# Kernel tuning notes

Hardware: AMD Instinct MI355X
Metric: run time of the kernel (lower is better)

The kernel has to match this reference:

```python
import jax, jax.numpy as jnp
import numpy as np

DEPTH = 4  # truncation depth from init_kwargs


def restricted_exp(dx, depth):
    # exp(dx) in truncated tensor algebra: level k = dx^{\otimes k} / k!
    terms = [dx]
    for k in range(2, depth + 1):
        terms.append(jnp.tensordot(terms[-1], dx, axes=0) / k)
    return tuple(terms)


def chen_mult(a, b, depth):
    # Chen's relation: c_k = a_k + b_k + sum_{i=1}^{k-1} a_i \otimes b_{k-i}
    out = []
    for k in range(1, depth + 1):
        term = a[k - 1] + b[k - 1]
        for i in range(1, k):
            term = term + jnp.tensordot(a[i - 1], b[k - i - 1], axes=0)
        out.append(term)
    return tuple(out)


def signature(path, depth):
    inc = path[1:] - path[:-1]  # [L-1, D] path increments
    carry0 = restricted_exp(inc[0], depth)

    def step(carry, dx):
        return chen_mult(carry, restricted_exp(dx, depth), depth), None

    sig, _ = jax.lax.scan(step, carry0, inc[1:])
    # flatten=True: concat levels 1..depth -> [D + D^2 + ... + D^depth]
    return jnp.concatenate([t.reshape(-1) for t in sig])


def setup_inputs() -> dict:
    key = jax.random.key(0)
    path = jax.random.normal(key, (8192, 8), dtype=jnp.float32)
    return {"path": path}


def reference(path):
    return signature(path, DEPTH)
```

## Files before the change

kernel.cpp:

```cpp
#include <hip/hip_runtime.h>

#define SIGLEN 4680
#define S1OFF 0
#define S2OFF 8
#define S3OFF 72
#define S4OFF 584
#define NCHUNK 256
#define NG 16
#define MAXLEN 128
#define LROW 592

struct SigRegs { float s4[16]; float a1, a2, a30, a31; };

__device__ __forceinline__ int s3off(int c) {
  return S3OFF + 4 * (c ^ ((c >> 4) & 7));
}

__device__ __forceinline__ void load_sig(SigRegs& A, const float* __restrict__ B,
                                         int i_idx, int t) {
  const float4* p4 = (const float4*)(B + S4OFF + 16 * t);
#pragma unroll
  for (int r = 0; r < 4; ++r) {
    const float4 v = p4[r];
    A.s4[4 * r] = v.x; A.s4[4 * r + 1] = v.y; A.s4[4 * r + 2] = v.z; A.s4[4 * r + 3] = v.w;
  }
  A.a1 = B[S1OFF + i_idx];
  A.a2 = B[S2OFF + (t >> 2)];
  const float2 a3i = *(const float2*)(B + S3OFF + 2 * t);
  A.a30 = a3i.x; A.a31 = a3i.y;
}

__device__ __forceinline__ void store_sig(const SigRegs& A, float* __restrict__ o,
                                          int i_idx, int t) {
  if ((t & 31) == 0) o[S1OFF + i_idx] = A.a1;
  if ((t & 3) == 0) o[S2OFF + (t >> 2)] = A.a2;
  *(float2*)(o + S3OFF + 2 * t) = make_float2(A.a30, A.a31);
  float4* o4 = (float4*)(o + S4OFF + 16 * t);
#pragma unroll
  for (int r = 0; r < 4; ++r)
    o4[r] = make_float4(A.s4[4 * r], A.s4[4 * r + 1], A.s4[4 * r + 2], A.s4[4 * r + 3]);
}

__device__ __forceinline__ void fold_lds(SigRegs& A, const float* __restrict__ R,
                                         const float4* __restrict__ q4,
                                         int i_idx, int j_idx, int k0, int t) {
  const float4 b1lo = *(const float4*)(R + S1OFF);
  const float4 b1hi = *(const float4*)(R + S1OFF + 4);
  const float b1i = R[S1OFF + i_idx];
  const float b1j = R[S1OFF + j_idx];
  const float2 b1k = *(const float2*)(R + S1OFF + k0);
  const float b2own = R[S2OFF + (t >> 2)];
  const float2 b2p = *(const float2*)(R + S2OFF + ((2 * t) & 63));
  const float2 b3p = *(const float2*)(R + s3off(t >> 1) + 2 * (t & 1));
  const float4* q2 = (const float4*)(R + S2OFF + 16 * (t & 3));
#pragma unroll
  for (int r = 0; r < 4; ++r) {
    const float4 v2 = q2[r];
    const float4 v3 = *(const float4*)(R + s3off(4 * (t & 31) + r));
    const float4 v4 = q4[r];
    const float a3v = (r < 2) ? A.a30 : A.a31;
    const float4 bb = (r & 1) ? b1hi : b1lo;
    A.s4[4 * r + 0] += v4.x + A.a1 * v3.x + A.a2 * v2.x + a3v * bb.x;
    A.s4[4 * r + 1] += v4.y + A.a1 * v3.y + A.a2 * v2.y + a3v * bb.y;
    A.s4[4 * r + 2] += v4.z + A.a1 * v3.z + A.a2 * v2.z + a3v * bb.z;
    A.s4[4 * r + 3] += v4.w + A.a1 * v3.w + A.a2 * v2.w + a3v * bb.w;
  }
  A.a30 += b3p.x + A.a1 * b2p.x + A.a2 * b1k.x;
  A.a31 += b3p.y + A.a1 * b2p.y + A.a2 * b1k.y;
  A.a2 += b2own + A.a1 * b1j;
  A.a1 += b1i;
}

__device__ __forceinline__ void loadq4(float4* dst, const float* __restrict__ gbase,
                                       int m, int t) {
  const float4* g = (const float4*)(gbase + (long)m * SIGLEN + S4OFF + 16 * t);
#pragma unroll
  for (int r = 0; r < 4; ++r) dst[r] = g[r];
}

__device__ __forceinline__ void fold16(const float* __restrict__ gbase,
                                       float* __restrict__ outp,
                                       float* __restrict__ lsig,
                                       int i_idx, int j_idx, int k0, int t) {
  SigRegs A;
  load_sig(A, gbase, i_idx, t);
  float4 qA[4], qB[4];
  loadq4(qA, gbase, 1, t);
  loadq4(qB, gbase, 2, t);

  {
    float4 vals[10];
#pragma unroll
    for (int s = 0; s < 10; ++s) {
      const int v = t + 256 * s;
      const int vc = (v < NG * 146) ? v : (NG * 146 - 1);
      const int sig = vc / 146;
      const int r = vc - sig * 146;
      vals[s] = *(const float4*)(gbase + (long)sig * SIGLEN + 4 * r);
    }
#pragma unroll
    for (int s = 0; s < 10; ++s) {
      const int v = t + 256 * s;
      if (v < NG * 146) {
        const int sig = v / 146;
        const int r = v - sig * 146;
        const int off = (r < 18) ? 4 * r : s3off(r - 18);
        *(float4*)(lsig + sig * LROW + off) = vals[s];
      }
    }
  }
  __syncthreads();

#pragma unroll 1
  for (int m = 1; m < NG - 2; m += 2) {
    fold_lds(A, lsig + m * LROW, qA, i_idx, j_idx, k0, t);
    loadq4(qA, gbase, m + 2, t);
    fold_lds(A, lsig + (m + 1) * LROW, qB, i_idx, j_idx, k0, t);
    if (m + 3 < NG) loadq4(qB, gbase, m + 3, t);
  }
  fold_lds(A, lsig + (NG - 1) * LROW, qA, i_idx, j_idx, k0, t);
  store_sig(A, outp, i_idx, t);
}

__global__ __launch_bounds__(256, 1) void sig_chunk(const float* __restrict__ path,
                                                    float* __restrict__ partials,
                                                    int nInc) {
  __shared__ float4 pl[(MAXLEN + 1) * 2];
  __shared__ float4 dv[MAXLEN * 2];
  const int t = threadIdx.x;
  const int c = blockIdx.x;
  const int i_idx = t >> 5;
  const int j_idx = (t >> 2) & 7;
  const int k0 = 2 * (t & 3);

  const long start = ((long)c * nInc) / NCHUNK;
  const long end = ((long)(c + 1) * nInc) / NCHUNK;
  const int len = (int)(end - start);

  const float4* gp = (const float4*)(path + start * 8);
  for (int idx = t; idx < (len + 1) * 2; idx += 256) pl[idx] = gp[idx];
  __syncthreads();
  for (int idx = t; idx < len * 2; idx += 256) {
    float4 a = pl[idx + 2], b = pl[idx];
    dv[idx] = make_float4(a.x - b.x, a.y - b.y, a.z - b.z, a.w - b.w);
  }
  __syncthreads();
  const float* dvf = (const float*)dv;

  SigRegs A;
#pragma unroll
  for (int e = 0; e < 16; ++e) A.s4[e] = 0.f;
  A.a1 = 0.f; A.a2 = 0.f; A.a30 = 0.f; A.a31 = 0.f;

  for (int it = 0; it < len; ++it) {
    const float4 d0 = dv[it * 2], d1 = dv[it * 2 + 1];
    const float dxl[8] = {d0.x, d0.y, d0.z, d0.w, d1.x, d1.y, d1.z, d1.w};
    const float dxi = dvf[it * 8 + i_idx];
    const float dxj = dvf[it * 8 + j_idx];
    const float2 dkk = *(const float2*)(dvf + it * 8 + k0);

    const float inner = 0.5f * A.a2 + dxj * ((1.f / 6.f) * A.a1 + (1.f / 24.f) * dxi);
    const float c0 = A.a30 + dkk.x * inner;
    const float c1 = A.a31 + dkk.y * inner;
#pragma unroll
    for (int l = 0; l < 8; ++l) A.s4[l] += c0 * dxl[l];
#pragma unroll
    for (int l = 0; l < 8; ++l) A.s4[8 + l] += c1 * dxl[l];
    const float common3 = A.a2 + dxj * (0.5f * A.a1 + (1.f / 6.f) * dxi);
    A.a30 += common3 * dkk.x;
    A.a31 += common3 * dkk.y;
    A.a2 += dxj * (A.a1 + 0.5f * dxi);
    A.a1 += dxi;
  }

  store_sig(A, partials + (long)c * SIGLEN, i_idx, t);
}

__global__ __launch_bounds__(256, 1) void sig_fold16(const float* __restrict__ in,
                                                     float* __restrict__ outp) {
  __shared__ float lsig[NG * LROW];
  const int t = threadIdx.x;
  const int b = blockIdx.x;
  const int i_idx = t >> 5;
  const int j_idx = (t >> 2) & 7;
  const int k0 = 2 * (t & 3);
  fold16(in + (long)(NG * b) * SIGLEN, outp + (long)b * SIGLEN, lsig,
         i_idx, j_idx, k0, t);
}

__global__ __launch_bounds__(256, 1) void sig_fold_final(const float* __restrict__ in,
                                                         float* __restrict__ outp) {
  __shared__ float lsig[NG * LROW];
  const int t = threadIdx.x;
  const int i_idx = t >> 5;
  const int j_idx = (t >> 2) & 7;
  const int k0 = 2 * (t & 3);
  fold16(in, outp, lsig, i_idx, j_idx, k0, t);
}

extern "C" void kernel_launch(void* const* d_in, const int* in_sizes, int n_in,
                              void* d_out, int out_size, void* d_ws, size_t ws_size,
                              hipStream_t stream) {
  const float* path = (const float*)d_in[0];
  float* out = (float*)d_out;
  const int L = in_sizes[0] / 8;
  const int nInc = L - 1;

  float* partials = (float*)d_ws;
  float* g2 = partials + (long)NCHUNK * SIGLEN;

  sig_chunk<<<NCHUNK, 256, 0, stream>>>(path, partials, nInc);
  sig_fold16<<<NG, 256, 0, stream>>>(partials, g2);
  sig_fold_final<<<1, 256, 0, stream>>>(g2, out);
}
```

Baseline: 28.42 us.

## Merge final fold into fold kernel via flag-based inter-block handoff

Replaces the separate final-fold launch with a single fold kernel: block 0 keeps its partial signature in registers, waits on per-block flags set by the other 15 blocks, then folds their results itself. This is meant to remove one kernel launch and its launch gap. Partial stores also switch to nontemporal stores. The flag spin-wait relies on all 16 blocks being co-resident, and the flags in workspace must start at zero; they are reset after use.

After: 34.34 us. +20.8%, slower.

```diff
diff --git a/kernel.cpp b/kernel.cpp
--- a/kernel.cpp
+++ b/kernel.cpp
@@ -7,8 +7,12 @@
 #define S4OFF 584
 #define NCHUNK 256
 #define NG 16
+#define MAGIC 0x13572468u
 #define MAXLEN 128
 #define LROW 592
+
+typedef float f4v __attribute__((ext_vector_type(4)));
+typedef float f2v __attribute__((ext_vector_type(2)));
 
 struct SigRegs { float s4[16]; float a1, a2, a30, a31; };
 
@@ -39,6 +43,28 @@
 #pragma unroll
   for (int r = 0; r < 4; ++r)
     o4[r] = make_float4(A.s4[4 * r], A.s4[4 * r + 1], A.s4[4 * r + 2], A.s4[4 * r + 3]);
+}
+
+__device__ __forceinline__ void store_sig_nt(const SigRegs& A, float* __restrict__ o,
+                                             int i_idx, int t) {
+  if ((t & 31) == 0) __builtin_nontemporal_store(A.a1, o + S1OFF + i_idx);
+  if ((t & 3) == 0) __builtin_nontemporal_store(A.a2, o + S2OFF + (t >> 2));
+  f2v v2; v2.x = A.a30; v2.y = A.a31;
+  __builtin_nontemporal_store(v2, (f2v*)(o + S3OFF + 2 * t));
+  f4v* o4 = (f4v*)(o + S4OFF + 16 * t);
+#pragma unroll
+  for (int r = 0; r < 4; ++r) {
+    f4v v; v.x = A.s4[4 * r]; v.y = A.s4[4 * r + 1];
+    v.z = A.s4[4 * r + 2]; v.w = A.s4[4 * r + 3];
+    __builtin_nontemporal_store(v, o4 + r);
+  }
+}
+
+__device__ __forceinline__ void wait_flag_relaxed(unsigned* f) {
+  for (long i = 0; i < 200000000L; ++i) {
+    if (__hip_atomic_load(f, __ATOMIC_RELAXED, __HIP_MEMORY_SCOPE_AGENT) == MAGIC)
+      return;
+  }
 }
 
 __device__ __forceinline__ void fold_lds(SigRegs& A, const float* __restrict__ R,
@@ -78,48 +104,44 @@
   for (int r = 0; r < 4; ++r) dst[r] = g[r];
 }
 
-__device__ __forceinline__ void fold16(const float* __restrict__ gbase,
-                                       float* __restrict__ outp,
-                                       float* __restrict__ lsig,
-                                       int i_idx, int j_idx, int k0, int t) {
-  SigRegs A;
-  load_sig(A, gbase, i_idx, t);
+__device__ __forceinline__ void stage_sigs(const float* __restrict__ gbase, int nsig,
+                                           float* __restrict__ lsig, int t) {
+  const int lim = nsig * 146;
+  float4 vals[10];
+#pragma unroll
+  for (int s = 0; s < 10; ++s) {
+    const int v = t + 256 * s;
+    const int vc = (v < lim) ? v : (lim - 1);
+    const int sig = vc / 146;
+    const int r = vc - sig * 146;
+    vals[s] = *(const float4*)(gbase + (long)sig * SIGLEN + 4 * r);
+  }
+#pragma unroll
+  for (int s = 0; s < 10; ++s) {
+    const int v = t + 256 * s;
+    if (v < lim) {
+      const int sig = v / 146;
+      const int r = v - sig * 146;
+      const int off = (r < 18) ? 4 * r : s3off(r - 18);
+      *(float4*)(lsig + sig * LROW + off) = vals[s];
+    }
+  }
+}
+
+__device__ __forceinline__ void fold_seq15(SigRegs& A, const float* __restrict__ gbase,
+                                           int s0, const float* __restrict__ lsig,
+                                           int r0, int i_idx, int j_idx, int k0, int t) {
   float4 qA[4], qB[4];
-  loadq4(qA, gbase, 1, t);
-  loadq4(qB, gbase, 2, t);
-
-  {
-    float4 vals[10];
-#pragma unroll
-    for (int s = 0; s < 10; ++s) {
-      const int v = t + 256 * s;
-      const int vc = (v < NG * 146) ? v : (NG * 146 - 1);
-      const int sig = vc / 146;
-      const int r = vc - sig * 146;
-      vals[s] = *(const float4*)(gbase + (long)sig * SIGLEN + 4 * r);
-    }
-#pragma unroll
-    for (int s = 0; s < 10; ++s) {
-      const int v = t + 256 * s;
-      if (v < NG * 146) {
-        const int sig = v / 146;
-        const int r = v - sig * 146;
-        const int off = (r < 18) ? 4 * r : s3off(r - 18);
-        *(float4*)(lsig + sig * LROW + off) = vals[s];
-      }
-    }
-  }
-  __syncthreads();
-
+  loadq4(qA, gbase, s0, t);
+  loadq4(qB, gbase, s0 + 1, t);
 #pragma unroll 1
-  for (int m = 1; m < NG - 2; m += 2) {
-    fold_lds(A, lsig + m * LROW, qA, i_idx, j_idx, k0, t);
-    loadq4(qA, gbase, m + 2, t);
-    fold_lds(A, lsig + (m + 1) * LROW, qB, i_idx, j_idx, k0, t);
-    if (m + 3 < NG) loadq4(qB, gbase, m + 3, t);
-  }
-  fold_lds(A, lsig + (NG - 1) * LROW, qA, i_idx, j_idx, k0, t);
-  store_sig(A, outp, i_idx, t);
+  for (int m = 0; m + 2 < 15; m += 2) {
+    fold_lds(A, lsig + (r0 + m) * LROW, qA, i_idx, j_idx, k0, t);
+    loadq4(qA, gbase, s0 + m + 2, t);
+    fold_lds(A, lsig + (r0 + m + 1) * LROW, qB, i_idx, j_idx, k0, t);
+    if (m + 3 < 15) loadq4(qB, gbase, s0 + m + 3, t);
+  }
+  fold_lds(A, lsig + (r0 + 14) * LROW, qA, i_idx, j_idx, k0, t);
 }
 
 __global__ __launch_bounds__(256, 1) void sig_chunk(const float* __restrict__ path,
@@ -173,29 +195,49 @@
     A.a1 += dxi;
   }
 
-  store_sig(A, partials + (long)c * SIGLEN, i_idx, t);
-}
-
-__global__ __launch_bounds__(256, 1) void sig_fold16(const float* __restrict__ in,
-                                                     float* __restrict__ outp) {
+  store_sig_nt(A, partials + (long)c * SIGLEN, i_idx, t);
+}
+
+__global__ __launch_bounds__(256, 1) void sig_fold(const float* __restrict__ partials,
+                                                   float* __restrict__ out,
+                                                   float* __restrict__ g2,
+                                                   unsigned* __restrict__ cflag) {
   __shared__ float lsig[NG * LROW];
   const int t = threadIdx.x;
   const int b = blockIdx.x;
   const int i_idx = t >> 5;
   const int j_idx = (t >> 2) & 7;
   const int k0 = 2 * (t & 3);
-  fold16(in + (long)(NG * b) * SIGLEN, outp + (long)b * SIGLEN, lsig,
-         i_idx, j_idx, k0, t);
-}
-
-__global__ __launch_bounds__(256, 1) void sig_fold_final(const float* __restrict__ in,
-                                                         float* __restrict__ outp) {
-  __shared__ float lsig[NG * LROW];
-  const int t = threadIdx.x;
-  const int i_idx = t >> 5;
-  const int j_idx = (t >> 2) & 7;
-  const int k0 = 2 * (t & 3);
-  fold16(in, outp, lsig, i_idx, j_idx, k0, t);
+
+  const float* gbase = partials + (long)(NG * b) * SIGLEN;
+  stage_sigs(gbase, NG, lsig, t);
+  SigRegs A;
+  load_sig(A, gbase, i_idx, t);
+  __syncthreads();
+  fold_seq15(A, gbase, 1, lsig, 1, i_idx, j_idx, k0, t);
+
+  if (b != 0) {
+    store_sig_nt(A, g2 + (long)b * SIGLEN, i_idx, t);
+    __syncthreads();
+    if (t == 0) {
+      __threadfence();
+      __hip_atomic_store(&cflag[b], MAGIC, __ATOMIC_RELAXED, __HIP_MEMORY_SCOPE_AGENT);
+    }
+    return;
+  }
+
+  if (t < NG - 1) wait_flag_relaxed(&cflag[t + 1]);
+  __syncthreads();
+  __builtin_amdgcn_fence(__ATOMIC_ACQUIRE, "agent");
+
+  stage_sigs(g2 + SIGLEN, NG - 1, lsig, t);
+  __syncthreads();
+  fold_seq15(A, g2 + SIGLEN, 0, lsig, 0, i_idx, j_idx, k0, t);
+
+  store_sig(A, out, i_idx, t);
+
+  __syncthreads();
+  if (t < NG - 1) cflag[t + 1] = 0u;
 }
 
 extern "C" void kernel_launch(void* const* d_in, const int* in_sizes, int n_in,
@@ -208,8 +250,8 @@
 
   float* partials = (float*)d_ws;
   float* g2 = partials + (long)NCHUNK * SIGLEN;
+  unsigned* cflag = (unsigned*)(g2 + (long)NG * SIGLEN);
 
   sig_chunk<<<NCHUNK, 256, 0, stream>>>(path, partials, nInc);
-  sig_fold16<<<NG, 256, 0, stream>>>(partials, g2);
-  sig_fold_final<<<1, 256, 0, stream>>>(g2, out);
-}
+  sig_fold<<<NG, 256, 0, stream>>>(partials, out, g2, cflag);
+}
```

## Use fewer, longer chunks and fold all partials in one kernel

Applied to the files above, without the earlier changes.

The path is now split into 64 chunks of about 128 increments instead of 256 chunks of 32. The two-stage fold (16 blocks of 16, then a final fold of 16) becomes one single-block kernel that stages all 63 remaining partial signatures in LDS through double-buffered loads and folds them serially. This drops one kernel launch and the intermediate global round trip. In exchange, each chunk block does a longer serial scan, the final fold has a longer serial dependency chain, and the fold kernel needs about 149KB of LDS.

After: 49.21 us. +73.1%, slower.

```diff
diff --git a/kernel.cpp b/kernel.cpp
--- a/kernel.cpp
+++ b/kernel.cpp
@@ -5,10 +5,11 @@
 #define S2OFF 8
 #define S3OFF 72
 #define S4OFF 584
-#define NCHUNK 256
-#define NG 16
+#define NCHUNK 64
 #define MAXLEN 128
 #define LROW 592
+#define NFOLD 63
+#define NCH4 (NFOLD * 146)
 
 struct SigRegs { float s4[16]; float a1, a2, a30, a31; };
 
@@ -78,50 +79,6 @@
   for (int r = 0; r < 4; ++r) dst[r] = g[r];
 }
 
-__device__ __forceinline__ void fold16(const float* __restrict__ gbase,
-                                       float* __restrict__ outp,
-                                       float* __restrict__ lsig,
-                                       int i_idx, int j_idx, int k0, int t) {
-  SigRegs A;
-  load_sig(A, gbase, i_idx, t);
-  float4 qA[4], qB[4];
-  loadq4(qA, gbase, 1, t);
-  loadq4(qB, gbase, 2, t);
-
-  {
-    float4 vals[10];
-#pragma unroll
-    for (int s = 0; s < 10; ++s) {
-      const int v = t + 256 * s;
-      const int vc = (v < NG * 146) ? v : (NG * 146 - 1);
-      const int sig = vc / 146;
-      const int r = vc - sig * 146;
-      vals[s] = *(const float4*)(gbase + (long)sig * SIGLEN + 4 * r);
-    }
-#pragma unroll
-    for (int s = 0; s < 10; ++s) {
-      const int v = t + 256 * s;
-      if (v < NG * 146) {
-        const int sig = v / 146;
-        const int r = v - sig * 146;
-        const int off = (r < 18) ? 4 * r : s3off(r - 18);
-        *(float4*)(lsig + sig * LROW + off) = vals[s];
-      }
-    }
-  }
-  __syncthreads();
-
-#pragma unroll 1
-  for (int m = 1; m < NG - 2; m += 2) {
-    fold_lds(A, lsig + m * LROW, qA, i_idx, j_idx, k0, t);
-    loadq4(qA, gbase, m + 2, t);
-    fold_lds(A, lsig + (m + 1) * LROW, qB, i_idx, j_idx, k0, t);
-    if (m + 3 < NG) loadq4(qB, gbase, m + 3, t);
-  }
-  fold_lds(A, lsig + (NG - 1) * LROW, qA, i_idx, j_idx, k0, t);
-  store_sig(A, outp, i_idx, t);
-}
-
 __global__ __launch_bounds__(256, 1) void sig_chunk(const float* __restrict__ path,
                                                     float* __restrict__ partials,
                                                     int nInc) {
@@ -176,26 +133,63 @@
   store_sig(A, partials + (long)c * SIGLEN, i_idx, t);
 }
 
-__global__ __launch_bounds__(256, 1) void sig_fold16(const float* __restrict__ in,
-                                                     float* __restrict__ outp) {
-  __shared__ float lsig[NG * LROW];
-  const int t = threadIdx.x;
-  const int b = blockIdx.x;
-  const int i_idx = t >> 5;
-  const int j_idx = (t >> 2) & 7;
-  const int k0 = 2 * (t & 3);
-  fold16(in + (long)(NG * b) * SIGLEN, outp + (long)b * SIGLEN, lsig,
-         i_idx, j_idx, k0, t);
-}
-
-__global__ __launch_bounds__(256, 1) void sig_fold_final(const float* __restrict__ in,
-                                                         float* __restrict__ outp) {
-  __shared__ float lsig[NG * LROW];
+__global__ __launch_bounds__(256, 1) void sig_fold_all(const float* __restrict__ partials,
+                                                       float* __restrict__ out) {
+  __shared__ float lsig[NFOLD * LROW];
   const int t = threadIdx.x;
   const int i_idx = t >> 5;
   const int j_idx = (t >> 2) & 7;
   const int k0 = 2 * (t & 3);
-  fold16(in, outp, lsig, i_idx, j_idx, k0, t);
+  const float* gb = partials + SIGLEN;
+
+#define LOADB(buf, k)                                                         \
+  _Pragma("unroll") for (int s = 0; s < 9; ++s) {                             \
+    const int g = t + 256 * (9 * (k) + s);                                    \
+    const int gc = (g < NCH4) ? g : (NCH4 - 1);                               \
+    const int sig = gc / 146;                                                 \
+    const int r = gc - sig * 146;                                             \
+    buf[s] = *(const float4*)(gb + (long)sig * SIGLEN + 4 * r);               \
+  }
+#define WRITEB(buf, k)                                                        \
+  _Pragma("unroll") for (int s = 0; s < 9; ++s) {                             \
+    const int g = t + 256 * (9 * (k) + s);                                    \
+    if (g < NCH4) {                                                           \
+      const int sig = g / 146;                                                \
+      const int r = g - sig * 146;                                            \
+      const int off = (r < 18) ? 4 * r : s3off(r - 18);                       \
+      *(float4*)(lsig + sig * LROW + off) = buf[s];                           \
+    }                                                                         \
+  }
+
+  float4 va[9], vb[9];
+  LOADB(va, 0);
+  LOADB(vb, 1);
+
+  SigRegs A;
+  load_sig(A, partials, i_idx, t);
+  float4 qA[4], qB[4];
+  loadq4(qA, gb, 0, t);
+  loadq4(qB, gb, 1, t);
+
+  WRITEB(va, 0);
+  LOADB(va, 2);
+  WRITEB(vb, 1);
+  LOADB(vb, 3);
+  WRITEB(va, 2);
+  WRITEB(vb, 3);
+#undef LOADB
+#undef WRITEB
+  __syncthreads();
+
+#pragma unroll 1
+  for (int m = 0; m + 2 < NFOLD; m += 2) {
+    fold_lds(A, lsig + m * LROW, qA, i_idx, j_idx, k0, t);
+    loadq4(qA, gb, m + 2, t);
+    fold_lds(A, lsig + (m + 1) * LROW, qB, i_idx, j_idx, k0, t);
+    if (m + 3 < NFOLD) loadq4(qB, gb, m + 3, t);
+  }
+  fold_lds(A, lsig + (NFOLD - 1) * LROW, qA, i_idx, j_idx, k0, t);
+  store_sig(A, out, i_idx, t);
 }
 
 extern "C" void kernel_launch(void* const* d_in, const int* in_sizes, int n_in,
@@ -207,9 +201,7 @@
   const int nInc = L - 1;
 
   float* partials = (float*)d_ws;
-  float* g2 = partials + (long)NCHUNK * SIGLEN;
 
   sig_chunk<<<NCHUNK, 256, 0, stream>>>(path, partials, nInc);
-  sig_fold16<<<NG, 256, 0, stream>>>(partials, g2);
-  sig_fold_final<<<1, 256, 0, stream>>>(g2, out);
-}
+  sig_fold_all<<<1, 256, 0, stream>>>(partials, out);
+}
```
